# Kernel optimization log

Hardware: AMD Instinct MI355X
Metric: run time of the kernel (lower is better)

The kernel has to match this reference:

```python
import jax, jax.numpy as jnp
import numpy as np

DIM = 1024
NUM_HEADS = 16
HEAD_DIM = DIM // NUM_HEADS


def setup_inputs() -> dict:
    key = jax.random.key(0)
    k_x, k_wqkv, k_bqkv, k_wo, k_bo = jax.random.split(key, 5)
    scale = DIM ** -0.5
    return {
        "x": jax.random.normal(k_x, (4, 2048, DIM), dtype=jnp.float32),
        "w_qkv": jax.random.normal(k_wqkv, (DIM, 3 * DIM), dtype=jnp.float32) * scale,
        "b_qkv": jax.random.normal(k_bqkv, (3 * DIM,), dtype=jnp.float32) * 0.02,
        "w_out": jax.random.normal(k_wo, (DIM, DIM), dtype=jnp.float32) * scale,
        "b_out": jax.random.normal(k_bo, (DIM,), dtype=jnp.float32) * 0.02,
    }


def reference(x, w_qkv, b_qkv, w_out, b_out):
    B, S, D = x.shape
    H, Hd = NUM_HEADS, HEAD_DIM
    # QKV projection: (B,S,3D) -> (3,B,H,S,Hd)
    qkv = (x @ w_qkv + b_qkv).reshape(B, S, 3, H, Hd).transpose(2, 0, 3, 1, 4)
    q, k, v = qkv[0], qkv[1], qkv[2]
    scores = jnp.einsum('bhqd,bhkd->bhqk', q, k) / (Hd ** 0.5)
    attn = jax.nn.softmax(scores, axis=-1)  # dropout is identity in eval
    out = jnp.einsum('bhqk,bhkd->bhqd', attn, v)
    out = out.transpose(0, 2, 1, 3).reshape(B, S, D)
    return out @ w_out + b_out
```

## Files before the change

kernel.cpp:

```cpp
#include <hip/hip_runtime.h>
#include <hip/hip_bf16.h>
#include <stdint.h>

#define SEQ 2048
#define DIM 1024
#define NH 16
#define HD 64

typedef __attribute__((ext_vector_type(8))) short short8;
typedef __attribute__((ext_vector_type(4))) float f32x4;
typedef __attribute__((ext_vector_type(4))) float float4v;
typedef __attribute__((ext_vector_type(4))) unsigned short u16x4;
typedef __attribute__((ext_vector_type(2))) unsigned int u32x2;

#define MFMA16(a, b, c) __builtin_amdgcn_mfma_f32_16x16x32_bf16(a, b, c, 0, 0, 0)

#define QSCALE 0.1803368801111244f
#define LOG2_THR 11.0f

__device__ __forceinline__ unsigned short f2b(float f) {
  union { float f; unsigned int u; } x; x.f = f;
  unsigned int r = (x.u + 0x7FFFu + ((x.u >> 16) & 1u)) >> 16;
  return (unsigned short)r;
}

__device__ __forceinline__ unsigned int pk2(float a, float b) {
  __hip_bfloat162 h = __float22bfloat162_rn(float2{a, b});
  union { __hip_bfloat162 h; unsigned int u; } c; c.h = h;
  return c.u;
}

__device__ __forceinline__ void gld16(const void* g, void* l) {
  __builtin_amdgcn_global_load_lds(
      (const __attribute__((address_space(1))) unsigned int*)(uintptr_t)g,
      (__attribute__((address_space(3))) unsigned int*)(unsigned int)(uintptr_t)l,
      16, 0, 0);
}

__global__ void cast_bf16_kernel(const float* __restrict__ in,
                                 unsigned short* __restrict__ out, int n4) {
  int stride = gridDim.x * blockDim.x;
  for (int i = blockIdx.x * blockDim.x + threadIdx.x; i < n4; i += stride) {
    float4v v = *(const float4v*)(in + (size_t)i * 4);
    u16x4 o;
    o.x = f2b(v.x); o.y = f2b(v.y); o.z = f2b(v.z); o.w = f2b(v.w);
    *(u16x4*)(out + (size_t)i * 4) = o;
  }
}

__global__ void transpose_cast_kernel(const float* __restrict__ in,
                                      unsigned short* __restrict__ out,
                                      int rows, int cols) {
  __shared__ float tile[32][33];
  const int t = threadIdx.x, tx = t & 31, ty = t >> 5;
  const int c0 = blockIdx.x * 32, r0 = blockIdx.y * 32;
#pragma unroll
  for (int j = 0; j < 4; j++)
    tile[ty + 8 * j][tx] = in[(size_t)(r0 + ty + 8 * j) * cols + c0 + tx];
  __syncthreads();
#pragma unroll
  for (int j = 0; j < 4; j++)
    out[(size_t)(c0 + ty + 8 * j) * rows + r0 + tx] = f2b(tile[tx][ty + 8 * j]);
}

template <int EPI>
__global__ __launch_bounds__(256, 2) void gemm_bt_kernel(
    const unsigned short* __restrict__ A, const unsigned short* __restrict__ Bt,
    const float* __restrict__ bias, float* __restrict__ Cf,
    int M, int N, int K,
    unsigned short* __restrict__ Qb, unsigned short* __restrict__ Kb,
    unsigned short* __restrict__ Vt) {
  __shared__ unsigned short lA[128 * 32];
  __shared__ unsigned short lB[128 * 32];
  const int t = threadIdx.x, lane = t & 63, w = t >> 6;
  const int l15 = lane & 15, lg = lane >> 4;
  const int wr = (w >> 1) * 64, wc = (w & 1) * 64;
  const int bm = blockIdx.x, bn = blockIdx.y;
  const char* Ag = (const char*)(A + (size_t)bm * 128 * K);
  const char* Bg = (const char*)(Bt + (size_t)bn * 128 * K);
  const int sr = t >> 2;
  const int sc = (t & 3) * 16;
  const size_t rowb = (size_t)K * 2;

  f32x4 acc[4][4];
#pragma unroll
  for (int m = 0; m < 4; m++)
#pragma unroll
    for (int n = 0; n < 4; n++) acc[m][n] = (f32x4){0.f, 0.f, 0.f, 0.f};

  for (int k0 = 0; k0 < K; k0 += 32) {
    __syncthreads();
    const size_t kbyte = (size_t)k0 * 2;
    gld16(Ag + (size_t)sr * rowb + kbyte + sc, &lA[t * 8]);
    gld16(Ag + (size_t)(sr + 64) * rowb + kbyte + sc, &lA[2048 + t * 8]);
    gld16(Bg + (size_t)sr * rowb + kbyte + sc, &lB[t * 8]);
    gld16(Bg + (size_t)(sr + 64) * rowb + kbyte + sc, &lB[2048 + t * 8]);
    asm volatile("s_waitcnt vmcnt(0)" ::: "memory");
    __syncthreads();
    short8 af[4], bf_[4];
#pragma unroll
    for (int m = 0; m < 4; m++)
      af[m] = *(const short8*)&lA[(wr + m * 16 + l15) * 32 + lg * 8];
#pragma unroll
    for (int n = 0; n < 4; n++)
      bf_[n] = *(const short8*)&lB[(wc + n * 16 + l15) * 32 + lg * 8];
#pragma unroll
    for (int m = 0; m < 4; m++)
#pragma unroll
      for (int n = 0; n < 4; n++)
        acc[m][n] = MFMA16(af[m], bf_[n], acc[m][n]);
  }

#pragma unroll
  for (int m = 0; m < 4; m++) {
#pragma unroll
    for (int n = 0; n < 4; n++) {
      const int row0 = bm * 128 + wr + m * 16 + lg * 4;
      const int col = bn * 128 + wc + n * 16 + l15;
      const float bv = bias[col];
#pragma unroll
      for (int rr = 0; rr < 4; rr++) {
        const float v = acc[m][n][rr] + bv;
        const int row = row0 + rr;
        if (EPI == 1) {
          Cf[(size_t)row * N + col] = v;
        } else {
          const int three = col >> 10, rem = col & 1023;
          const int h = rem >> 6, d = rem & 63;
          const int b = row >> 11, s = row & 2047;
          const size_t bh = (size_t)(b * NH + h);
          if (three == 0)
            Qb[(bh * SEQ + s) * HD + d] = f2b(v * QSCALE);
          else if (three == 1)
            Kb[(bh * SEQ + s) * HD + d] = f2b(v);
          else
            Vt[(bh * HD + d) * SEQ + s] = f2b(v);
        }
      }
    }
  }
}

__global__ __launch_bounds__(256, 3) void attn_kernel(
    const unsigned short* __restrict__ Qb, const unsigned short* __restrict__ Kb,
    const unsigned short* __restrict__ Vt, unsigned short* __restrict__ AO) {
  __shared__ unsigned short kT[2][64 * 64];
  __shared__ unsigned short vT[2][64 * 64];
  __shared__ unsigned short pT[4][32 * 64];
  const int t = threadIdx.x, lane = t & 63, w = t >> 6;
  const int l15 = lane & 15, lg = lane >> 4;
  const int q0 = blockIdx.x * 128;
  const int bh = blockIdx.y;
  const char* Qg = (const char*)(Qb + (size_t)bh * SEQ * HD);
  const char* Kg = (const char*)(Kb + (size_t)bh * SEQ * HD);
  const char* Vg = (const char*)(Vt + (size_t)bh * HD * SEQ);

  short8 qa[2][2];
#pragma unroll
  for (int h = 0; h < 2; h++) {
    const char* qrow = Qg + (size_t)(q0 + w * 32 + h * 16 + l15) * 128;
    qa[h][0] = *(const short8*)(qrow + lg * 16);
    qa[h][1] = *(const short8*)(qrow + 64 + lg * 16);
  }

  f32x4 o[2][4];
#pragma unroll
  for (int h = 0; h < 2; h++)
#pragma unroll
    for (int n = 0; n < 4; n++) o[h][n] = (f32x4){0.f, 0.f, 0.f, 0.f};
  float m_r[2] = {-1e30f, -1e30f}, l_r[2] = {0.f, 0.f};

  const int sr0 = t >> 3;
  const int scx = (t & 7) * 16;

#define STAGE(buf, kv0_)                                                               \
  do {                                                                                 \
    const int r0_ = sr0, r1_ = sr0 + 32;                                               \
    gld16(Kg + (size_t)((kv0_) + r0_) * 128 + (scx ^ ((r0_ & 7) << 4)),                \
          &kT[buf][t * 8]);                                                            \
    gld16(Kg + (size_t)((kv0_) + r1_) * 128 + (scx ^ ((r1_ & 7) << 4)),                \
          &kT[buf][2048 + t * 8]);                                                     \
    gld16(Vg + (size_t)r0_ * (SEQ * 2) + (size_t)(kv0_) * 2 + (scx ^ ((r0_ & 7) << 4)),\
          &vT[buf][t * 8]);                                                            \
    gld16(Vg + (size_t)r1_ * (SEQ * 2) + (size_t)(kv0_) * 2 + (scx ^ ((r1_ & 7) << 4)),\
          &vT[buf][2048 + t * 8]);                                                     \
  } while (0)

  STAGE(0, 0);
  asm volatile("s_waitcnt vmcnt(0)" ::: "memory");
  __syncthreads();
  int cur = 0;

  for (int kv0 = 0; kv0 < SEQ; kv0 += 64) {
    if (kv0 + 64 < SEQ) STAGE(cur ^ 1, kv0 + 64);

    const char* kb = (const char*)&kT[cur][0];
    f32x4 s[2][4];
#pragma unroll
    for (int h = 0; h < 2; h++)
#pragma unroll
      for (int n = 0; n < 4; n++) s[h][n] = (f32x4){0.f, 0.f, 0.f, 0.f};
    __builtin_amdgcn_s_setprio(1);
#pragma unroll
    for (int n = 0; n < 4; n++) {
      const int row = n * 16 + l15;
      const char* kr = kb + row * 128;
      const int sw = (row & 7) << 4;
      short8 a0 = *(const short8*)(kr + ((lg * 16) ^ sw));
      short8 a1 = *(const short8*)(kr + ((64 + lg * 16) ^ sw));
      s[0][n] = MFMA16(a0, qa[0][0], s[0][n]);
      s[0][n] = MFMA16(a1, qa[0][1], s[0][n]);
      s[1][n] = MFMA16(a0, qa[1][0], s[1][n]);
      s[1][n] = MFMA16(a1, qa[1][1], s[1][n]);
    }
    __builtin_amdgcn_s_setprio(0);

    float mx[2];
#pragma unroll
    for (int h = 0; h < 2; h++) {
      float m0 = fmaxf(fmaxf(s[h][0][0], s[h][0][1]), fmaxf(s[h][0][2], s[h][0][3]));
#pragma unroll
      for (int n = 1; n < 4; n++) {
        m0 = fmaxf(m0, fmaxf(fmaxf(s[h][n][0], s[h][n][1]), fmaxf(s[h][n][2], s[h][n][3])));
      }
      m0 = fmaxf(m0, __shfl_xor(m0, 16, 64));
      m0 = fmaxf(m0, __shfl_xor(m0, 32, 64));
      mx[h] = m0;
    }

    const int grow = (mx[0] > m_r[0] + LOG2_THR) | (mx[1] > m_r[1] + LOG2_THR);
    if (__any(grow)) {
      float al[2];
#pragma unroll
      for (int h = 0; h < 2; h++) {
        const float nm = fmaxf(m_r[h], mx[h]);
        al[h] = exp2f(m_r[h] - nm);
        m_r[h] = nm;
        l_r[h] *= al[h];
      }
#pragma unroll
      for (int h = 0; h < 2; h++)
#pragma unroll
        for (int r = 0; r < 4; r++) {
          const float alb = __shfl(al[h], lg * 4 + r, 64);
#pragma unroll
          for (int n = 0; n < 4; n++) o[h][n][r] *= alb;
        }
    }

    char* pb = (char*)&pT[w][0];
    const int swp = (l15 & 7) << 4;
#pragma unroll
    for (int h = 0; h < 2; h++) {
      float rs = 0.f;
#pragma unroll
      for (int n = 0; n < 4; n++) {
#pragma unroll
        for (int r = 0; r < 4; r++) {
          const float p = exp2f(s[h][n][r] - m_r[h]);
          s[h][n][r] = p;
          rs += p;
        }
        u32x2 c;
        c.x = pk2(s[h][n][0], s[h][n][1]);
        c.y = pk2(s[h][n][2], s[h][n][3]);
        *(u32x2*)(pb + (h * 16 + l15) * 128 + ((n * 32 + lg * 8) ^ swp)) = c;
      }
      rs += __shfl_xor(rs, 16, 64);
      rs += __shfl_xor(rs, 32, 64);
      l_r[h] += rs;
    }
    short8 pa[2][2];
#pragma unroll
    for (int h = 0; h < 2; h++) {
      const char* pr = pb + (h * 16 + l15) * 128;
      pa[h][0] = *(const short8*)(pr + ((lg * 16) ^ swp));
      pa[h][1] = *(const short8*)(pr + ((64 + lg * 16) ^ swp));
    }

    const char* vb = (const char*)&vT[cur][0];
    __builtin_amdgcn_s_setprio(1);
#pragma unroll
    for (int n = 0; n < 4; n++) {
      const int row = n * 16 + l15;
      const char* vr = vb + row * 128;
      const int sw = (row & 7) << 4;
      short8 b0 = *(const short8*)(vr + ((lg * 16) ^ sw));
      short8 b1 = *(const short8*)(vr + ((64 + lg * 16) ^ sw));
      o[0][n] = MFMA16(pa[0][0], b0, o[0][n]);
      o[0][n] = MFMA16(pa[0][1], b1, o[0][n]);
      o[1][n] = MFMA16(pa[1][0], b0, o[1][n]);
      o[1][n] = MFMA16(pa[1][1], b1, o[1][n]);
    }
    __builtin_amdgcn_s_setprio(0);

    asm volatile("s_waitcnt vmcnt(0)" ::: "memory");
    __syncthreads();
    cur ^= 1;
  }
#undef STAGE

  float inv[2];
#pragma unroll
  for (int h = 0; h < 2; h++) inv[h] = 1.f / l_r[h];
  const int b = bh >> 4, hh = bh & 15;
  unsigned short* aob = AO + (size_t)b * SEQ * DIM + (size_t)hh * HD;
#pragma unroll
  for (int h = 0; h < 2; h++)
#pragma unroll
    for (int r = 0; r < 4; r++) {
      const float lb = __shfl(inv[h], lg * 4 + r, 64);
      const int s_ = q0 + w * 32 + h * 16 + lg * 4 + r;
#pragma unroll
      for (int n = 0; n < 4; n++) {
        const int d_ = n * 16 + l15;
        aob[(size_t)s_ * DIM + d_] = f2b(o[h][n][r] * lb);
      }
    }
}

extern "C" void kernel_launch(void* const* d_in, const int* in_sizes, int n_in,
                              void* d_out, int out_size, void* d_ws, size_t ws_size,
                              hipStream_t stream) {
  const float* x = (const float*)d_in[0];
  const float* w_qkv = (const float*)d_in[1];
  const float* b_qkv = (const float*)d_in[2];
  const float* w_out = (const float*)d_in[3];
  const float* b_out = (const float*)d_in[4];
  float* out = (float*)d_out;

  char* ws = (char*)d_ws;
  unsigned short* xb    = (unsigned short*)(ws);
  unsigned short* wqkvT = (unsigned short*)(ws + (16u << 20));
  unsigned short* woT   = (unsigned short*)(ws + (22u << 20));
  unsigned short* Qb    = (unsigned short*)(ws + (24u << 20));
  unsigned short* Kb    = (unsigned short*)(ws + (40u << 20));
  unsigned short* Vt    = (unsigned short*)(ws + (56u << 20));
  unsigned short* AO    = (unsigned short*)(ws + (72u << 20));

  const int M = 4 * SEQ;

  cast_bf16_kernel<<<2048, 256, 0, stream>>>(x, xb, M * DIM / 4);
  transpose_cast_kernel<<<dim3(3 * DIM / 32, DIM / 32), 256, 0, stream>>>(w_qkv, wqkvT, DIM, 3 * DIM);
  transpose_cast_kernel<<<dim3(DIM / 32, DIM / 32), 256, 0, stream>>>(w_out, woT, DIM, DIM);

  gemm_bt_kernel<0><<<dim3(M / 128, 3 * DIM / 128), 256, 0, stream>>>(
      xb, wqkvT, b_qkv, nullptr, M, 3 * DIM, DIM, Qb, Kb, Vt);

  attn_kernel<<<dim3(SEQ / 128, 4 * NH), 256, 0, stream>>>(Qb, Kb, Vt, AO);

  gemm_bt_kernel<1><<<dim3(M / 128, DIM / 128), 256, 0, stream>>>(
      AO, woT, b_out, out, M, DIM, DIM, nullptr, nullptr, nullptr);
}
```

Before: 329.8 us.

## Use raw v_exp_f32, XCD-aware attention block mapping, vectorized V-transpose stores

Replaces exp2f with inline v_exp_f32, which drops the range-handling code the library exp2f wraps around the hardware instruction. Remaps the attention grid so that all query blocks of a given batch-head land on the same XCD, which should improve L2 reuse of K/V. Restructures the QKV GEMM epilogue so the transposed V is written as packed 4-element stores instead of scattered 2-byte stores. The raw exp skips denormal handling, which is harmless here because inputs are always at or below zero.

```diff
diff --git a/kernel.cpp b/kernel.cpp
--- a/kernel.cpp
+++ b/kernel.cpp
@@ -22,6 +22,12 @@
   union { float f; unsigned int u; } x; x.f = f;
   unsigned int r = (x.u + 0x7FFFu + ((x.u >> 16) & 1u)) >> 16;
   return (unsigned short)r;
+}
+
+__device__ __forceinline__ float exp2v(float x) {
+  float r;
+  asm("v_exp_f32 %0, %1" : "=v"(r) : "v"(x));
+  return r;
 }
 
 __device__ __forceinline__ unsigned int pk2(float a, float b) {
@@ -118,23 +124,28 @@
       const int row0 = bm * 128 + wr + m * 16 + lg * 4;
       const int col = bn * 128 + wc + n * 16 + l15;
       const float bv = bias[col];
-#pragma unroll
-      for (int rr = 0; rr < 4; rr++) {
-        const float v = acc[m][n][rr] + bv;
-        const int row = row0 + rr;
-        if (EPI == 1) {
-          Cf[(size_t)row * N + col] = v;
+      if (EPI == 1) {
+#pragma unroll
+        for (int rr = 0; rr < 4; rr++)
+          Cf[(size_t)(row0 + rr) * N + col] = acc[m][n][rr] + bv;
+      } else {
+        const int three = col >> 10, rem = col & 1023;
+        const int h = rem >> 6, d = rem & 63;
+        const int b = row0 >> 11, s0 = row0 & 2047;
+        const size_t bh = (size_t)(b * NH + h);
+        if (three == 0) {
+#pragma unroll
+          for (int rr = 0; rr < 4; rr++)
+            Qb[(bh * SEQ + s0 + rr) * HD + d] = f2b((acc[m][n][rr] + bv) * QSCALE);
+        } else if (three == 1) {
+#pragma unroll
+          for (int rr = 0; rr < 4; rr++)
+            Kb[(bh * SEQ + s0 + rr) * HD + d] = f2b(acc[m][n][rr] + bv);
         } else {
-          const int three = col >> 10, rem = col & 1023;
-          const int h = rem >> 6, d = rem & 63;
-          const int b = row >> 11, s = row & 2047;
-          const size_t bh = (size_t)(b * NH + h);
-          if (three == 0)
-            Qb[(bh * SEQ + s) * HD + d] = f2b(v * QSCALE);
-          else if (three == 1)
-            Kb[(bh * SEQ + s) * HD + d] = f2b(v);
-          else
-            Vt[(bh * HD + d) * SEQ + s] = f2b(v);
+          u16x4 pk;
+#pragma unroll
+          for (int rr = 0; rr < 4; rr++) pk[rr] = f2b(acc[m][n][rr] + bv);
+          *(u16x4*)&Vt[(bh * HD + d) * SEQ + s0] = pk;
         }
       }
     }
@@ -149,8 +160,10 @@
   __shared__ unsigned short pT[4][32 * 64];
   const int t = threadIdx.x, lane = t & 63, w = t >> 6;
   const int l15 = lane & 15, lg = lane >> 4;
-  const int q0 = blockIdx.x * 128;
-  const int bh = blockIdx.y;
+  const int flat = blockIdx.y * 16 + blockIdx.x;
+  const int xcd = flat & 7, j = flat >> 3;
+  const int bh = xcd * 8 + (j >> 4);
+  const int q0 = (j & 15) * 128;
   const char* Qg = (const char*)(Qb + (size_t)bh * SEQ * HD);
   const char* Kg = (const char*)(Kb + (size_t)bh * SEQ * HD);
   const char* Vg = (const char*)(Vt + (size_t)bh * HD * SEQ);
@@ -234,7 +247,7 @@
 #pragma unroll
       for (int h = 0; h < 2; h++) {
         const float nm = fmaxf(m_r[h], mx[h]);
-        al[h] = exp2f(m_r[h] - nm);
+        al[h] = exp2v(m_r[h] - nm);
         m_r[h] = nm;
         l_r[h] *= al[h];
       }
@@ -257,7 +270,7 @@
       for (int n = 0; n < 4; n++) {
 #pragma unroll
         for (int r = 0; r < 4; r++) {
-          const float p = exp2f(s[h][n][r] - m_r[h]);
+          const float p = exp2v(s[h][n][r] - m_r[h]);
           s[h][n][r] = p;
           rs += p;
         }
```

Measured after the change: 300.7 us. -8.8%, faster.
